# Kernel tuning notes

Hardware: AMD Instinct MI355X
Metric: run time of the kernel (lower is better)

Reference implementation:

```python
import jax, jax.numpy as jnp
import numpy as np

B, T, N, F = 4096, 64, 8, 4
H = 64           # GRU hidden
EID = 16         # id embedding dim
CM = 32          # comm message dim
D = H + EID + CM # 112, attention dim
INV_SQRT_D = 1.0 / np.sqrt(112.0)


def setup_inputs() -> dict:
    key = jax.random.key(0)
    ks = jax.random.split(key, 24)
    def rn(k, shape, s=0.05):
        return jax.random.normal(k, shape, jnp.float32) * s
    return {
        "seq": jax.random.normal(ks[0], (B, T, N, F), jnp.float32),
        # GRU (torch layout: W_ih [3H,F], W_hh [3H,H], gates ordered r,z,n)
        "W_ih": rn(ks[1], (3 * H, F)), "W_hh": rn(ks[2], (3 * H, H)),
        "b_ih": rn(ks[3], (3 * H,)), "b_hh": rn(ks[4], (3 * H,)),
        "embed": rn(ks[5], (8, EID)),
        "Wm": rn(ks[6], (CM, H + EID)), "bm": rn(ks[7], (CM,)),
        "Wq": rn(ks[8], (D, D)), "bq": rn(ks[9], (D,)),
        "Wk": rn(ks[10], (D, D)), "bk": rn(ks[11], (D,)),
        "Wv": rn(ks[12], (D, D)), "bv": rn(ks[13], (D,)),
        "W1": rn(ks[14], (128, D)), "b1": rn(ks[15], (128,)),
        "W2": rn(ks[16], (128, 128)), "b2": rn(ks[17], (128,)),
        "Wmean": rn(ks[18], (2, 128)), "bmean": rn(ks[19], (2,)),
        "Wval": rn(ks[20], (1, 128)), "bval": rn(ks[21], (1,)),
    }


def _policy(seq, W_ih, W_hh, b_ih, b_hh, embed, Wm, bm,
            Wq, bq, Wk, bk, Wv, bv, W1, b1, W2, b2, Wmean, bmean, Wval, bval):
    Bb, Tt, Nn, Ff = seq.shape
    # Faithful to torch: raw view [B,T,N,F] -> [B*N,T,F] (no permute)
    x = seq.reshape(Bb * Nn, Tt, Ff)
    # Precompute all input-to-hidden projections once: [BN, T, 3H]
    x_proj = jnp.einsum('btf,gf->btg', x, W_ih) + b_ih

    def step(h, xp):
        gh = h @ W_hh.T + b_hh
        xr, xz, xn = jnp.split(xp, 3, axis=-1)
        hr, hz, hn = jnp.split(gh, 3, axis=-1)
        r = jax.nn.sigmoid(xr + hr)
        z = jax.nn.sigmoid(xz + hz)
        n = jnp.tanh(xn + r * hn)
        return (1.0 - z) * n + z * h, None

    h0 = jnp.zeros((Bb * Nn, H), seq.dtype)
    hT, _ = jax.lax.scan(step, h0, jnp.swapaxes(x_proj, 0, 1))  # carry == out[:, -1]
    h = hT.reshape(Bb, Nn, H)

    id_emb = jnp.broadcast_to(embed[:Nn], (Bb, Nn, EID))
    msgs = jnp.concatenate([h, id_emb], axis=-1) @ Wm.T + bm      # [B,N,32]
    c = jnp.broadcast_to(msgs.mean(axis=1, keepdims=True), (Bb, Nn, CM))
    h = jnp.concatenate([h, id_emb, c], axis=-1)                   # [B,N,112]

    Q = h @ Wq.T + bq
    K = h @ Wk.T + bk
    V = h @ Wv.T + bv
    attn = jax.nn.softmax(jnp.einsum('bnd,bmd->bnm', Q, K) * INV_SQRT_D, axis=-1)
    h = jnp.einsum('bnm,bmd->bnd', attn, V)

    h = jax.nn.relu(h @ W1.T + b1)
    h = jax.nn.relu(h @ W2.T + b2)
    return (h @ Wmean.T + bmean, h @ Wval.T + bval)


def reference(seq, W_ih, W_hh, b_ih, b_hh, embed, Wm, bm,
              Wq, bq, Wk, bk, Wv, bv, W1, b1, W2, b2, Wmean, bmean, Wval, bval):
    return _policy(seq, W_ih, W_hh, b_ih, b_hh, embed, Wm, bm,
                   Wq, bq, Wk, bk, Wv, bv, W1, b1, W2, b2,
                   Wmean, bmean, Wval, bval)
```

## Files before the change

kernel.cpp:

```cpp
#include <hip/hip_runtime.h>


typedef float f32x4 __attribute__((ext_vector_type(4)));
typedef short bf16x8 __attribute__((ext_vector_type(8)));

#define MFMA16 __builtin_amdgcn_mfma_f32_16x16x32_bf16
#define LOG2E 1.44269504088896f
#define INV_SQRT_D 0.09449111825230679f

__device__ __forceinline__ short f2bf(float f) {
    union { float f; unsigned u; } v; v.f = f;
    unsigned r = v.u + 0x7fffu + ((v.u >> 16) & 1u);
    return (short)(r >> 16);
}
__device__ __forceinline__ short f2bf_hu(float f) {
    union { float f; unsigned u; } v; v.f = f;
    return (short)((v.u + 0x8000u) >> 16);
}
__device__ __forceinline__ float fexp2(float x) { return __builtin_amdgcn_exp2f(x); }
__device__ __forceinline__ float frcp(float x)  { return __builtin_amdgcn_rcpf(x); }
__device__ __forceinline__ void lds_fence() {
    __asm__ __volatile__("s_waitcnt lgkmcnt(0)" ::: "memory");
}

__global__ void conv_kernel(
    const float* __restrict__ Wm, const float* __restrict__ Wq,
    const float* __restrict__ Wk, const float* __restrict__ Wv,
    const float* __restrict__ W1, const float* __restrict__ W2,
    const float* __restrict__ Wmean, const float* __restrict__ Wval,
    unsigned short* __restrict__ wf)
{
    int gid = blockIdx.x * 256 + threadIdx.x;
    if (gid >= 158 * 64) return;
    int fid = gid >> 6, lane = gid & 63;
    int l15 = lane & 15, q = lane >> 4;

    short out[8] = {0,0,0,0,0,0,0,0};
    if (fid < 154) {
        const float* W; int nrows, Klim, idx;
        if (fid < 6)        { W = Wm; nrows = 32;  Klim = 80;  idx = fid;       }
        else if (fid < 34)  { W = Wq; nrows = 112; Klim = 112; idx = fid - 6;   }
        else if (fid < 62)  { W = Wk; nrows = 112; Klim = 112; idx = fid - 34;  }
        else if (fid < 90)  { W = Wv; nrows = 112; Klim = 112; idx = fid - 62;  }
        else if (fid < 122) { W = W1; nrows = 128; Klim = 112; idx = fid - 90;  }
        else                { W = W2; nrows = 128; Klim = 128; idx = fid - 122; }
        int nch = (fid < 6) ? 3 : 4;
        int ct = idx / nch, ch = idx - ct * nch;
        int g = ct * 16 + l15, k0 = ch * 32 + q * 8;
        if (g < nrows && (k0 + 8) <= Klim) {
            const float* wp = W + (size_t)g * Klim + k0;
            #pragma unroll
            for (int u = 0; u < 8; ++u) out[u] = f2bf(wp[u]);
        }
    } else {
        int ch = fid - 154, k0 = ch * 32 + q * 8;
        const float* wp = (l15 == 0) ? Wmean : (l15 == 1) ? (Wmean + 128)
                          : (l15 == 2) ? Wval : nullptr;
        if (wp) {
            #pragma unroll
            for (int u = 0; u < 8; ++u) out[u] = f2bf(wp[k0 + u]);
        }
    }
    *(bf16x8*)(wf + ((size_t)fid * 64 + lane) * 8) = *(bf16x8*)out;
}

__global__ __launch_bounds__(256, 1)
void policy_kernel(
    const float* __restrict__ seq,
    const float* __restrict__ W_ih, const float* __restrict__ W_hh,
    const float* __restrict__ b_ih, const float* __restrict__ b_hh,
    const float* __restrict__ embed,
    const unsigned short* __restrict__ wf,
    const float* __restrict__ bm, const float* __restrict__ bq,
    const float* __restrict__ bk, const float* __restrict__ bv,
    const float* __restrict__ b1, const float* __restrict__ b2,
    const float* __restrict__ bmean, const float* __restrict__ bval,
    float* __restrict__ out)
{
    __shared__ short R1s[4][16][136];
    __shared__ short R2s[4][16][136];
    __shared__ short R3s[4][16][136];
    __shared__ short Vts[4][114][20];
    __shared__ short Pbs[4][16][40];

    const int tid  = threadIdx.x;
    const int wv   = tid >> 6;
    const int lane = tid & 63;
    const int l15  = lane & 15;
    const int q    = lane >> 4;
    const int seqbase = (blockIdx.x * 4 + wv) * 16;

    short (*R1)[136] = R1s[wv];
    short (*R2)[136] = R2s[wv];
    short (*R3)[136] = R3s[wv];
    short (*Vt)[20]  = Vts[wv];
    short (*Pb)[40]  = Pbs[wv];
    const f32x4 zz = {0.f, 0.f, 0.f, 0.f};

    {
        int* p;
        p = (int*)&R1[0][0]; for (int i = lane; i < 1088; i += 64) p[i] = 0;
        p = (int*)&R2[0][0]; for (int i = lane; i < 1088; i += 64) p[i] = 0;
        p = (int*)&R3[0][0]; for (int i = lane; i < 1088; i += 64) p[i] = 0;
        p = (int*)&Vt[0][0]; for (int i = lane; i < 1140; i += 64) p[i] = 0;
        p = (int*)&Pb[0][0]; for (int i = lane; i < 320;  i += 64) p[i] = 0;
    }
    {
        int row = lane >> 2, j0 = (lane & 3) * 4;
        f32x4 e = *(const f32x4*)(embed + (row & 7) * 16 + j0);
        #pragma unroll
        for (int u = 0; u < 4; ++u) R1[row][64 + j0 + u] = f2bf(e[u]);
    }

    const float sc_rz = -LOG2E;
    const float sc_n  = 2.0f * LOG2E;
    bf16x8 Bh[12][2], B2[8], B2x[4];
    float bhh_n[4];
    #pragma unroll
    for (int j = 0; j < 12; ++j) {
        int g = j * 16 + l15;
        float s = (j < 8) ? sc_rz : sc_n;
        #pragma unroll
        for (int c = 0; c < 2; ++c) {
            const float* wp = W_hh + g * 64 + c * 32 + q * 8;
            bf16x8 f;
            #pragma unroll
            for (int u = 0; u < 8; ++u) f[u] = f2bf(wp[u] * s);
            Bh[j][c] = f;
        }
    }
    #pragma unroll
    for (int j = 0; j < 8; ++j) {
        int g = j * 16 + l15;
        bf16x8 f2 = {0,0,0,0,0,0,0,0};
        if (q == 0) {
            #pragma unroll
            for (int u = 0; u < 4; ++u) f2[u] = f2bf(W_ih[g * 4 + u] * sc_rz);
            f2[4] = f2bf((b_ih[g] + b_hh[g]) * sc_rz);
        }
        B2[j] = f2;
    }
    #pragma unroll
    for (int j2 = 0; j2 < 4; ++j2) {
        int g = 128 + j2 * 16 + l15;
        bf16x8 f = {0,0,0,0,0,0,0,0};
        if (q == 0) {
            #pragma unroll
            for (int u = 0; u < 4; ++u) f[u] = f2bf(W_ih[g * 4 + u] * sc_n);
            f[4] = f2bf(b_ih[g] * sc_n);
        }
        B2x[j2] = f;
        bhh_n[j2] = b_hh[g] * sc_n;
    }
    lds_fence();

    const short onebf = 0x3f80;
    float h[4][4];
    #pragma unroll
    for (int j = 0; j < 4; ++j)
        #pragma unroll
        for (int r = 0; r < 4; ++r) h[j][r] = 0.f;

    f32x4 xc = *(const f32x4*)(seq + (size_t)(seqbase + l15) * 256);

    for (int t = 0; t < 64; ++t) {
        int tn = (t < 63) ? t + 1 : 63;
        f32x4 xnext = *(const f32x4*)(seq + (size_t)(seqbase + l15) * 256 + tn * 4);

        bf16x8 A0 = *(const bf16x8*)&R1[l15][q * 8];
        bf16x8 A1 = *(const bf16x8*)&R1[l15][32 + q * 8];
        bf16x8 A2;
        A2[0] = f2bf_hu(xc[0]); A2[1] = f2bf_hu(xc[1]);
        A2[2] = f2bf_hu(xc[2]); A2[3] = f2bf_hu(xc[3]);
        A2[4] = onebf; A2[5] = 0; A2[6] = 0; A2[7] = 0;

        #pragma unroll
        for (int j = 0; j < 4; ++j) {
            f32x4 ar = MFMA16(A2, B2[j], zz, 0, 0, 0);
            ar = MFMA16(A0, Bh[j][0], ar, 0, 0, 0);
            ar = MFMA16(A1, Bh[j][1], ar, 0, 0, 0);
            f32x4 az = MFMA16(A2, B2[4 + j], zz, 0, 0, 0);
            az = MFMA16(A0, Bh[4 + j][0], az, 0, 0, 0);
            az = MFMA16(A1, Bh[4 + j][1], az, 0, 0, 0);
            f32x4 an = MFMA16(A0, Bh[8 + j][0], zz, 0, 0, 0);
            an = MFMA16(A1, Bh[8 + j][1], an, 0, 0, 0);
            f32x4 ax = MFMA16(A2, B2x[j], zz, 0, 0, 0);

            #pragma unroll
            for (int r = 0; r < 4; ++r) {
                float e_r  = fexp2(ar[r]);
                float rg   = frcp(1.f + e_r);
                float e_z  = fexp2(az[r]);
                float anb  = an[r] + bhh_n[j];
                float npre = fmaf(rg, anb, ax[r]);
                float e_t  = fexp2(npre);
                float tp   = e_t + 1.f;
                float tm   = e_t - 1.f;
                float hv   = h[j][r];
                float num  = fmaf(hv, tp, e_z * tm);
                float den  = fmaf(tp, e_z, tp);
                float hnew = num * frcp(den);
                h[j][r] = hnew;
                R1[q * 4 + r][16 * j + l15] = f2bf_hu(hnew);
            }
        }
        xc = xnext;
    }
    lds_fence();

    auto ld = [&](int fid) -> bf16x8 {
        return *(const bf16x8*)(wf + ((size_t)fid * 64 + lane) * 8);
    };

    #pragma unroll
    for (int ct = 0; ct < 2; ++ct) {
        f32x4 acc = zz;
        #pragma unroll
        for (int ch = 0; ch < 3; ++ch) {
            bf16x8 a = *(const bf16x8*)&R1[l15][ch * 32 + q * 8];
            acc = MFMA16(a, ld(ct * 3 + ch), acc, 0, 0, 0);
        }
        float s = acc[0] + acc[1] + acc[2] + acc[3];
        s += __shfl_xor(s, 16, 64);
        float cv = 0.125f * s + bm[16 * ct + l15];
        short cb = f2bf_hu(cv);
        #pragma unroll
        for (int r = 0; r < 4; ++r) R1[q * 4 + r][80 + 16 * ct + l15] = cb;
    }
    lds_fence();

    #pragma unroll
    for (int ct = 0; ct < 7; ++ct) {
        f32x4 aq = zz, ak = zz, av = zz;
        #pragma unroll
        for (int ch = 0; ch < 4; ++ch) {
            bf16x8 a = *(const bf16x8*)&R1[l15][ch * 32 + q * 8];
            aq = MFMA16(a, ld(6  + ct * 4 + ch), aq, 0, 0, 0);
            ak = MFMA16(a, ld(34 + ct * 4 + ch), ak, 0, 0, 0);
            av = MFMA16(a, ld(62 + ct * 4 + ch), av, 0, 0, 0);
        }
        int col = 16 * ct + l15;
        float biq = bq[col], bik = bk[col], biv = bv[col];
        #pragma unroll
        for (int r = 0; r < 4; ++r) {
            int row = q * 4 + r;
            R2[row][col] = f2bf_hu((aq[r] + biq) * INV_SQRT_D);
            R3[row][col] = f2bf_hu(ak[r] + bik);
            Vt[col][row] = f2bf_hu(av[r] + biv);
        }
    }
    lds_fence();

    {
        f32x4 acc = zz;
        #pragma unroll
        for (int ch = 0; ch < 4; ++ch) {
            bf16x8 a = *(const bf16x8*)&R2[l15][ch * 32 + q * 8];
            bf16x8 b = *(const bf16x8*)&R3[l15][ch * 32 + q * 8];
            acc = MFMA16(a, b, acc, 0, 0, 0);
        }
        bool collow = (l15 < 8);
        #pragma unroll
        for (int r = 0; r < 4; ++r) {
            int rl = q * 4 + r;
            bool valid = ((rl < 8) == collow);
            float v = acc[r];
            float m = v;
            m = fmaxf(m, __shfl_xor(m, 1, 64));
            m = fmaxf(m, __shfl_xor(m, 2, 64));
            m = fmaxf(m, __shfl_xor(m, 4, 64));
            float e = fexp2(LOG2E * (v - m));
            float s = e;
            s += __shfl_xor(s, 1, 64);
            s += __shfl_xor(s, 2, 64);
            s += __shfl_xor(s, 4, 64);
            float pv = valid ? e * frcp(s) : 0.f;
            Pb[rl][l15] = f2bf_hu(pv);
        }
    }
    lds_fence();

    {
        bf16x8 a = *(const bf16x8*)&Pb[l15][q * 8];
        #pragma unroll
        for (int ct = 0; ct < 7; ++ct) {
            bf16x8 b = *(const bf16x8*)&Vt[16 * ct + l15][q * 8];
            f32x4 acc = MFMA16(a, b, zz, 0, 0, 0);
            #pragma unroll
            for (int r = 0; r < 4; ++r) R1[q * 4 + r][16 * ct + l15] = f2bf_hu(acc[r]);
        }
    }
    lds_fence();

    #pragma unroll
    for (int ct = 0; ct < 8; ++ct) {
        f32x4 acc = zz;
        #pragma unroll
        for (int ch = 0; ch < 4; ++ch) {
            bf16x8 a = *(const bf16x8*)&R1[l15][ch * 32 + q * 8];
            acc = MFMA16(a, ld(90 + ct * 4 + ch), acc, 0, 0, 0);
        }
        float bias = b1[16 * ct + l15];
        #pragma unroll
        for (int r = 0; r < 4; ++r)
            R2[q * 4 + r][16 * ct + l15] = f2bf_hu(fmaxf(acc[r] + bias, 0.f));
    }
    lds_fence();

    #pragma unroll
    for (int ct = 0; ct < 8; ++ct) {
        f32x4 acc = zz;
        #pragma unroll
        for (int ch = 0; ch < 4; ++ch) {
            bf16x8 a = *(const bf16x8*)&R2[l15][ch * 32 + q * 8];
            acc = MFMA16(a, ld(122 + ct * 4 + ch), acc, 0, 0, 0);
        }
        float bias = b2[16 * ct + l15];
        #pragma unroll
        for (int r = 0; r < 4; ++r)
            R3[q * 4 + r][16 * ct + l15] = f2bf_hu(fmaxf(acc[r] + bias, 0.f));
    }
    lds_fence();

    {
        f32x4 acc = zz;
        #pragma unroll
        for (int ch = 0; ch < 4; ++ch) {
            bf16x8 a = *(const bf16x8*)&R3[l15][ch * 32 + q * 8];
            acc = MFMA16(a, ld(154 + ch), acc, 0, 0, 0);
        }
        if (l15 < 3) {
            float bias = (l15 == 0) ? bmean[0] : (l15 == 1) ? bmean[1] : bval[0];
            #pragma unroll
            for (int r = 0; r < 4; ++r) {
                int A = seqbase + q * 4 + r;
                float v = acc[r] + bias;
                if (l15 < 2) out[(size_t)A * 2 + l15] = v;
                else         out[65536 + A] = v;
            }
        }
    }
}

extern "C" void kernel_launch(void* const* d_in, const int* in_sizes, int n_in,
                              void* d_out, int out_size, void* d_ws, size_t ws_size,
                              hipStream_t stream) {
    const float* seq   = (const float*)d_in[0];
    const float* W_ih  = (const float*)d_in[1];
    const float* W_hh  = (const float*)d_in[2];
    const float* b_ih  = (const float*)d_in[3];
    const float* b_hh  = (const float*)d_in[4];
    const float* embed = (const float*)d_in[5];
    const float* Wm    = (const float*)d_in[6];
    const float* bm    = (const float*)d_in[7];
    const float* Wq    = (const float*)d_in[8];
    const float* bq    = (const float*)d_in[9];
    const float* Wk    = (const float*)d_in[10];
    const float* bk    = (const float*)d_in[11];
    const float* Wv    = (const float*)d_in[12];
    const float* bv    = (const float*)d_in[13];
    const float* W1    = (const float*)d_in[14];
    const float* b1    = (const float*)d_in[15];
    const float* W2    = (const float*)d_in[16];
    const float* b2    = (const float*)d_in[17];
    const float* Wmean = (const float*)d_in[18];
    const float* bmean = (const float*)d_in[19];
    const float* Wval  = (const float*)d_in[20];
    const float* bval  = (const float*)d_in[21];

    unsigned short* wf = (unsigned short*)d_ws;

    conv_kernel<<<40, 256, 0, stream>>>(Wm, Wq, Wk, Wv, W1, W2, Wmean, Wval, wf);
    policy_kernel<<<512, 256, 0, stream>>>(seq, W_ih, W_hh, b_ih, b_hh, embed, wf,
                                           bm, bq, bk, bv, b1, b2, bmean, bval,
                                           (float*)d_out);
}
```

Baseline: 270.4 us.

## Raise policy kernel to two blocks per CU by cutting registers and LDS

The launch bound changes from one to two blocks per CU so that more waves can hide latency in the serial GRU loop. To fit, the input-projection MFMA operands (B2/B2x) move out of per-lane registers into a shared LDS table built once by wave 0. They are re-read each timestep through an asm 'launder' so the compiler cannot hoist them back into registers. The separate V-transpose buffer is removed: V is computed after the softmax and stored into the now-free R2 region, which lowers LDS use. The cost is extra LDS reads on every GRU step, a block-wide barrier, and possible register spills under the tighter limit.

```diff
diff --git a/kernel.cpp b/kernel.cpp
--- a/kernel.cpp
+++ b/kernel.cpp
@@ -21,6 +21,10 @@
 __device__ __forceinline__ float frcp(float x)  { return __builtin_amdgcn_rcpf(x); }
 __device__ __forceinline__ void lds_fence() {
     __asm__ __volatile__("s_waitcnt lgkmcnt(0)" ::: "memory");
+}
+__device__ __forceinline__ int launder(int x) {
+    __asm__ __volatile__("" : "+v"(x));
+    return x;
 }
 
 __global__ void conv_kernel(
@@ -64,7 +68,7 @@
     *(bf16x8*)(wf + ((size_t)fid * 64 + lane) * 8) = *(bf16x8*)out;
 }
 
-__global__ __launch_bounds__(256, 1)
+__global__ __launch_bounds__(256, 2)
 void policy_kernel(
     const float* __restrict__ seq,
     const float* __restrict__ W_ih, const float* __restrict__ W_hh,
@@ -80,8 +84,8 @@
     __shared__ short R1s[4][16][136];
     __shared__ short R2s[4][16][136];
     __shared__ short R3s[4][16][136];
-    __shared__ short Vts[4][114][20];
     __shared__ short Pbs[4][16][40];
+    __shared__ short C2[12][64][8];
 
     const int tid  = threadIdx.x;
     const int wv   = tid >> 6;
@@ -93,16 +97,17 @@
     short (*R1)[136] = R1s[wv];
     short (*R2)[136] = R2s[wv];
     short (*R3)[136] = R3s[wv];
-    short (*Vt)[20]  = Vts[wv];
     short (*Pb)[40]  = Pbs[wv];
     const f32x4 zz = {0.f, 0.f, 0.f, 0.f};
+
+    const float sc_rz = -LOG2E;
+    const float sc_n  = 2.0f * LOG2E;
 
     {
         int* p;
         p = (int*)&R1[0][0]; for (int i = lane; i < 1088; i += 64) p[i] = 0;
         p = (int*)&R2[0][0]; for (int i = lane; i < 1088; i += 64) p[i] = 0;
         p = (int*)&R3[0][0]; for (int i = lane; i < 1088; i += 64) p[i] = 0;
-        p = (int*)&Vt[0][0]; for (int i = lane; i < 1140; i += 64) p[i] = 0;
         p = (int*)&Pb[0][0]; for (int i = lane; i < 320;  i += 64) p[i] = 0;
     }
     {
@@ -112,9 +117,32 @@
         for (int u = 0; u < 4; ++u) R1[row][64 + j0 + u] = f2bf(e[u]);
     }
 
-    const float sc_rz = -LOG2E;
-    const float sc_n  = 2.0f * LOG2E;
-    bf16x8 Bh[12][2], B2[8], B2x[4];
+    if (wv == 0) {
+        #pragma unroll
+        for (int j = 0; j < 8; ++j) {
+            int g = j * 16 + l15;
+            short f2[8] = {0,0,0,0,0,0,0,0};
+            if (q == 0) {
+                #pragma unroll
+                for (int u = 0; u < 4; ++u) f2[u] = f2bf(W_ih[g * 4 + u] * sc_rz);
+                f2[4] = f2bf((b_ih[g] + b_hh[g]) * sc_rz);
+            }
+            *(bf16x8*)&C2[j][lane][0] = *(bf16x8*)f2;
+        }
+        #pragma unroll
+        for (int j2 = 0; j2 < 4; ++j2) {
+            int g = 128 + j2 * 16 + l15;
+            short f2[8] = {0,0,0,0,0,0,0,0};
+            if (q == 0) {
+                #pragma unroll
+                for (int u = 0; u < 4; ++u) f2[u] = f2bf(W_ih[g * 4 + u] * sc_n);
+                f2[4] = f2bf(b_ih[g] * sc_n);
+            }
+            *(bf16x8*)&C2[8 + j2][lane][0] = *(bf16x8*)f2;
+        }
+    }
+
+    bf16x8 Bh[12][2];
     float bhh_n[4];
     #pragma unroll
     for (int j = 0; j < 12; ++j) {
@@ -130,29 +158,10 @@
         }
     }
     #pragma unroll
-    for (int j = 0; j < 8; ++j) {
-        int g = j * 16 + l15;
-        bf16x8 f2 = {0,0,0,0,0,0,0,0};
-        if (q == 0) {
-            #pragma unroll
-            for (int u = 0; u < 4; ++u) f2[u] = f2bf(W_ih[g * 4 + u] * sc_rz);
-            f2[4] = f2bf((b_ih[g] + b_hh[g]) * sc_rz);
-        }
-        B2[j] = f2;
-    }
-    #pragma unroll
-    for (int j2 = 0; j2 < 4; ++j2) {
-        int g = 128 + j2 * 16 + l15;
-        bf16x8 f = {0,0,0,0,0,0,0,0};
-        if (q == 0) {
-            #pragma unroll
-            for (int u = 0; u < 4; ++u) f[u] = f2bf(W_ih[g * 4 + u] * sc_n);
-            f[4] = f2bf(b_ih[g] * sc_n);
-        }
-        B2x[j2] = f;
-        bhh_n[j2] = b_hh[g] * sc_n;
-    }
-    lds_fence();
+    for (int j2 = 0; j2 < 4; ++j2)
+        bhh_n[j2] = b_hh[128 + j2 * 16 + l15] * sc_n;
+
+    __syncthreads();
 
     const short onebf = 0x3f80;
     float h[4][4];
@@ -161,6 +170,7 @@
         #pragma unroll
         for (int r = 0; r < 4; ++r) h[j][r] = 0.f;
 
+    const short* C2base = &C2[0][0][0];
     f32x4 xc = *(const f32x4*)(seq + (size_t)(seqbase + l15) * 256);
 
     for (int t = 0; t < 64; ++t) {
@@ -176,15 +186,19 @@
 
         #pragma unroll
         for (int j = 0; j < 4; ++j) {
-            f32x4 ar = MFMA16(A2, B2[j], zz, 0, 0, 0);
+            bf16x8 c2r = *(const bf16x8*)(C2base + launder(((j    ) * 64 + lane) * 8));
+            bf16x8 c2z = *(const bf16x8*)(C2base + launder(((4 + j) * 64 + lane) * 8));
+            bf16x8 c2n = *(const bf16x8*)(C2base + launder(((8 + j) * 64 + lane) * 8));
+
+            f32x4 ar = MFMA16(A2, c2r, zz, 0, 0, 0);
             ar = MFMA16(A0, Bh[j][0], ar, 0, 0, 0);
             ar = MFMA16(A1, Bh[j][1], ar, 0, 0, 0);
-            f32x4 az = MFMA16(A2, B2[4 + j], zz, 0, 0, 0);
+            f32x4 az = MFMA16(A2, c2z, zz, 0, 0, 0);
             az = MFMA16(A0, Bh[4 + j][0], az, 0, 0, 0);
             az = MFMA16(A1, Bh[4 + j][1], az, 0, 0, 0);
             f32x4 an = MFMA16(A0, Bh[8 + j][0], zz, 0, 0, 0);
             an = MFMA16(A1, Bh[8 + j][1], an, 0, 0, 0);
-            f32x4 ax = MFMA16(A2, B2x[j], zz, 0, 0, 0);
+            f32x4 ax = MFMA16(A2, c2n, zz, 0, 0, 0);
 
             #pragma unroll
             for (int r = 0; r < 4; ++r) {
@@ -231,22 +245,20 @@
 
     #pragma unroll
     for (int ct = 0; ct < 7; ++ct) {
-        f32x4 aq = zz, ak = zz, av = zz;
+        f32x4 aq = zz, ak = zz;
         #pragma unroll
         for (int ch = 0; ch < 4; ++ch) {
             bf16x8 a = *(const bf16x8*)&R1[l15][ch * 32 + q * 8];
             aq = MFMA16(a, ld(6  + ct * 4 + ch), aq, 0, 0, 0);
             ak = MFMA16(a, ld(34 + ct * 4 + ch), ak, 0, 0, 0);
-            av = MFMA16(a, ld(62 + ct * 4 + ch), av, 0, 0, 0);
         }
         int col = 16 * ct + l15;
-        float biq = bq[col], bik = bk[col], biv = bv[col];
+        float biq = bq[col], bik = bk[col];
         #pragma unroll
         for (int r = 0; r < 4; ++r) {
             int row = q * 4 + r;
             R2[row][col] = f2bf_hu((aq[r] + biq) * INV_SQRT_D);
             R3[row][col] = f2bf_hu(ak[r] + bik);
-            Vt[col][row] = f2bf_hu(av[r] + biv);
         }
     }
     lds_fence();
@@ -281,10 +293,30 @@
     lds_fence();
 
     {
+        short* VtR = &R2[0][0];
+        #pragma unroll
+        for (int ct = 0; ct < 7; ++ct) {
+            f32x4 av = zz;
+            #pragma unroll
+            for (int ch = 0; ch < 4; ++ch) {
+                bf16x8 a = *(const bf16x8*)&R1[l15][ch * 32 + q * 8];
+                av = MFMA16(a, ld(62 + ct * 4 + ch), av, 0, 0, 0);
+            }
+            int col = 16 * ct + l15;
+            float biv = bv[col];
+            #pragma unroll
+            for (int r = 0; r < 4; ++r)
+                VtR[col * 18 + q * 4 + r] = f2bf_hu(av[r] + biv);
+        }
+    }
+    lds_fence();
+
+    {
+        const short* VtR = &R2[0][0];
         bf16x8 a = *(const bf16x8*)&Pb[l15][q * 8];
         #pragma unroll
         for (int ct = 0; ct < 7; ++ct) {
-            bf16x8 b = *(const bf16x8*)&Vt[16 * ct + l15][q * 8];
+            bf16x8 b = *(const bf16x8*)(VtR + (16 * ct + l15) * 18 + q * 8);
             f32x4 acc = MFMA16(a, b, zz, 0, 0, 0);
             #pragma unroll
             for (int r = 0; r < 4; ++r) R1[q * 4 + r][16 * ct + l15] = f2bf_hu(acc[r]);
```

Result: faster. 236.2 us (-12.7%).
